# Kernel tuning notes

Hardware: AMD Instinct MI355X
Metric: run time of the kernel (lower is better)

The kernel has to match this reference:

```python
import jax, jax.numpy as jnp
import numpy as np

DIM = 1024
NUM_HEADS = 16
HEAD_DIM = DIM // NUM_HEADS
BATCH = 4
SEQ = 2048
EPS = 1e-6


def rotate_half(x):
    # interleaved-pair rotation: (..., d) -> view (..., d//2, 2), swap with sign
    x = x.reshape(*x.shape[:-1], -1, 2)
    x1, x2 = jnp.split(x, 2, axis=-1)  # each (..., d//2, 1)
    x = jnp.concatenate([-x2, x1], axis=-1)
    return x.reshape(*x.shape[:-2], -1)


def apply_rope(x, cos, sin):
    # x: [B,S,H,D], cos/sin: [S,D]
    cos = cos[None, :, None, :].astype(x.dtype)
    sin = sin[None, :, None, :].astype(x.dtype)
    return x * cos + rotate_half(x) * sin


def rms_norm(x, w):
    var = jnp.mean(jnp.square(x), axis=-1, keepdims=True)
    return x * jax.lax.rsqrt(var + EPS) * w


def setup_inputs() -> dict:
    key = jax.random.key(0)
    ks = jax.random.split(key, 8)
    s = 0.02
    return {
        "x": jax.random.normal(ks[0], (BATCH, SEQ, DIM), jnp.float32),
        "rope_cos": jnp.cos(jnp.arange(SEQ, dtype=jnp.float32)[:, None] *
                            (1.0 / (10000.0 ** (jnp.repeat(jnp.arange(HEAD_DIM // 2, dtype=jnp.float32), 2) * 2 / HEAD_DIM)))[None, :]),
        "rope_sin": jnp.sin(jnp.arange(SEQ, dtype=jnp.float32)[:, None] *
                            (1.0 / (10000.0 ** (jnp.repeat(jnp.arange(HEAD_DIM // 2, dtype=jnp.float32), 2) * 2 / HEAD_DIM)))[None, :]),
        "qkv_w": jax.random.normal(ks[1], (3 * DIM, DIM), jnp.float32) * s,
        "qkv_b": jax.random.normal(ks[2], (3 * DIM,), jnp.float32) * s,
        "proj_w": jax.random.normal(ks[3], (DIM, DIM), jnp.float32) * s,
        "proj_b": jax.random.normal(ks[4], (DIM,), jnp.float32) * s,
        "q_norm_w": jnp.ones((HEAD_DIM,), jnp.float32),
        "k_norm_w": jnp.ones((HEAD_DIM,), jnp.float32),
    }


def reference(x, rope_cos, rope_sin, qkv_w, qkv_b, proj_w, proj_b, q_norm_w, k_norm_w):
    B, S, C = x.shape
    H, D = NUM_HEADS, HEAD_DIM
    qkv = x @ qkv_w.T + qkv_b                      # [B,S,3C]
    qkv = qkv.reshape(B, S, 3, H, D)
    q, k, v = qkv[:, :, 0], qkv[:, :, 1], qkv[:, :, 2]  # [B,S,H,D]
    q = apply_rope(rms_norm(q, q_norm_w), rope_cos, rope_sin)
    k = apply_rope(rms_norm(k, k_norm_w), rope_cos, rope_sin)
    scale = 1.0 / np.sqrt(D).astype(np.float32)
    attn = jnp.einsum('bqhd,bkhd->bhqk', q.astype(jnp.float32), k.astype(jnp.float32))
    attn = jax.nn.softmax(attn * scale, axis=-1).astype(x.dtype)
    out = jnp.einsum('bhqk,bkhd->bqhd', attn, v).reshape(B, S, C)
    return out @ proj_w.T + proj_b
```

## Files before the change

### kernel.cpp

```cpp
#include <hip/hip_runtime.h>
#include <math.h>
#include <type_traits>

#define DIM 1024
#define NH 16
#define HD 64
#define BATCH 4
#define SEQ 2048
#define EPS 1e-6f

typedef __attribute__((ext_vector_type(8))) short short8;
typedef __attribute__((ext_vector_type(4))) short short4v;
typedef __attribute__((ext_vector_type(4))) float float4v;

__device__ inline unsigned short f2bf(float f) {
    unsigned u = __float_as_uint(f);
    u += 0x7FFF + ((u >> 16) & 1);
    return (unsigned short)(u >> 16);
}
__device__ inline float bf2f(unsigned short b) {
    return __uint_as_float(((unsigned)b) << 16);
}
__device__ inline unsigned pk2bf(float lo, float hi) {
    unsigned ul = __float_as_uint(lo) + 0x8000u;
    unsigned uh = __float_as_uint(hi) + 0x8000u;
    return __builtin_amdgcn_perm(uh, ul, 0x07060302u);
}
__device__ inline unsigned short hu2bf(float f) {
    return (unsigned short)((__float_as_uint(f) + 0x8000u) >> 16);
}

#if __has_builtin(__builtin_amdgcn_mfma_f32_16x16x16bf16_1k)
__device__ inline float4v mfma16(short4v a, short4v b, float4v c) {
    return __builtin_amdgcn_mfma_f32_16x16x16bf16_1k(a, b, c, 0, 0, 0);
}
#elif __has_builtin(__builtin_amdgcn_mfma_f32_16x16x16_bf16)
__device__ inline float4v mfma16(short4v a, short4v b, float4v c) {
    return __builtin_amdgcn_mfma_f32_16x16x16_bf16(a, b, c, 0, 0, 0);
}
#else
__device__ inline float4v mfma16(short4v a, short4v b, float4v c) {
    asm volatile("v_mfma_f32_16x16x16_bf16 %0, %1, %2, %0\n\ts_nop 4"
                 : "+v"(c) : "v"(a), "v"(b));
    return c;
}
#endif

#define GLDS16(gp, lp) __builtin_amdgcn_global_load_lds( \
    (const __attribute__((address_space(1))) void*)(gp), \
    (__attribute__((address_space(3))) void*)(lp), 16, 0, 0)

__global__ __launch_bounds__(256) void cast_f32_bf16(
    const float* __restrict__ src, unsigned short* __restrict__ dst, int n4)
{
    int i = blockIdx.x * 256 + threadIdx.x;
    if (i >= n4) return;
    float4 f = ((const float4*)src)[i];
    ushort4 o;
    o.x = f2bf(f.x); o.y = f2bf(f.y); o.z = f2bf(f.z); o.w = f2bf(f.w);
    ((ushort4*)dst)[i] = o;
}

__global__ __launch_bounds__(256) void prep_cs(
    const float* __restrict__ cos_t, const float* __restrict__ sin_t,
    unsigned* __restrict__ csT)
{
    int tid = blockIdx.x * 256 + threadIdx.x;
    int d = tid & 63, s = tid >> 6;
    float c = cos_t[s * 64 + d], sn = sin_t[s * 64 + d];
    csT[d * SEQ + s] = ((unsigned)f2bf(sn) << 16) | f2bf(c);
}

__global__ __launch_bounds__(256) void gemm_qkv_fused(
    const unsigned short* __restrict__ A, const unsigned short* __restrict__ W,
    const float* __restrict__ bias, const unsigned* __restrict__ csT,
    const float* __restrict__ qw, const float* __restrict__ kw,
    unsigned short* __restrict__ q, unsigned short* __restrict__ k,
    unsigned short* __restrict__ vt)
{
    __shared__ __align__(16) unsigned short As[128 * 32];
    __shared__ __align__(16) unsigned short Bs[128 * 32];

    const int t    = threadIdx.x;
    const int lane = t & 63;
    const int w    = t >> 6;
    const int row0 = blockIdx.y * 128;
    const int col0 = blockIdx.x * 128;
    const int wr   = (w & 1) * 64;
    const int wc   = (w >> 1) * 64;
    const int cl   = lane & 15;
    const int quad = lane >> 4;

    float4v acc[4][4];
#pragma unroll
    for (int i = 0; i < 4; ++i)
#pragma unroll
        for (int j = 0; j < 4; ++j) acc[i][j] = (float4v){0.f, 0.f, 0.f, 0.f};

    const int off1 = t * 16, off2 = 4096 + t * 16;
    const int r1 = off1 >> 6, c1 = off1 & 63;
    const int r2 = off2 >> 6, c2 = off2 & 63;
    const char* Ab = (const char*)A + (long)row0 * DIM * 2;
    const char* Wb = (const char*)W + (long)col0 * DIM * 2;
    const long  ks = DIM * 2;

    for (int k0 = 0; k0 < DIM; k0 += 32) {
        const long kb = (long)k0 * 2;
        GLDS16(Ab + (long)r1 * ks + kb + c1, (char*)As + off1);
        GLDS16(Ab + (long)r2 * ks + kb + c2, (char*)As + off2);
        GLDS16(Wb + (long)r1 * ks + kb + c1, (char*)Bs + off1);
        GLDS16(Wb + (long)r2 * ks + kb + c2, (char*)Bs + off2);
        __syncthreads();

        short8 af[4], bfr[4];
#pragma unroll
        for (int i = 0; i < 4; ++i)
            af[i] = *(const short8*)&As[(wr + i * 16 + cl) * 32 + quad * 8];
#pragma unroll
        for (int j = 0; j < 4; ++j)
            bfr[j] = *(const short8*)&Bs[(wc + j * 16 + cl) * 32 + quad * 8];
#pragma unroll
        for (int i = 0; i < 4; ++i)
#pragma unroll
            for (int j = 0; j < 4; ++j)
                acc[i][j] = __builtin_amdgcn_mfma_f32_16x16x32_bf16(af[i], bfr[j], acc[i][j], 0, 0, 0);
        __syncthreads();
    }

    const int gcol  = col0 + wc;
    const int b     = row0 >> 11;
    const int srow0 = (row0 & 2047) + wr;

    float bj[4];
#pragma unroll
    for (int j = 0; j < 4; ++j) bj[j] = bias[gcol + j * 16 + cl];

    if (gcol < 2 * DIM) {
        const bool isq = (gcol < DIM);
        const int  h   = (isq ? gcol : gcol - DIM) >> 6;
        const float* nw = isq ? qw : kw;
        const float scale = isq ? 0.125f : 1.0f;
        unsigned short* dst = (isq ? q : k) + ((long)(b * NH + h) * SEQ) * 64;

#pragma unroll
        for (int i = 0; i < 4; ++i)
#pragma unroll
            for (int j = 0; j < 4; ++j)
#pragma unroll
                for (int r = 0; r < 4; ++r) acc[i][j][r] += bj[j];

        float rinv[4][4];
#pragma unroll
        for (int i = 0; i < 4; ++i)
#pragma unroll
            for (int r = 0; r < 4; ++r) {
                float ss = acc[i][0][r] * acc[i][0][r];
                ss = fmaf(acc[i][1][r], acc[i][1][r], ss);
                ss = fmaf(acc[i][2][r], acc[i][2][r], ss);
                ss = fmaf(acc[i][3][r], acc[i][3][r], ss);
                ss += __shfl_xor(ss, 1, 64);
                ss += __shfl_xor(ss, 2, 64);
                ss += __shfl_xor(ss, 4, 64);
                ss += __shfl_xor(ss, 8, 64);
                rinv[i][r] = rsqrtf(ss * (1.f / 64.f) + EPS) * scale;
            }

        float nwj[4];
#pragma unroll
        for (int j = 0; j < 4; ++j) nwj[j] = nw[j * 16 + cl];

#pragma unroll
        for (int i = 0; i < 4; ++i) {
            const int sb = srow0 + i * 16 + quad * 4;
#pragma unroll
            for (int j = 0; j < 4; ++j) {
                const int d = j * 16 + cl;
                uint4 u4 = *(const uint4*)(csT + (long)d * SEQ + sb);
#pragma unroll
                for (int r = 0; r < 4; ++r) {
                    float qn = acc[i][j][r] * rinv[i][r] * nwj[j];
                    float p  = __shfl_xor(qn, 1, 64);
                    float pr = (cl & 1) ? p : -p;
                    unsigned u = (r == 0) ? u4.x : (r == 1) ? u4.y : (r == 2) ? u4.z : u4.w;
                    float c  = bf2f((unsigned short)(u & 0xffff));
                    float sn = bf2f((unsigned short)(u >> 16));
                    float ov = fmaf(qn, c, pr * sn);
                    dst[(long)(sb + r) * 64 + d] = hu2bf(ov);
                }
            }
        }
    } else {
        const int h = (gcol - 2 * DIM) >> 6;
        unsigned short* vdst = vt + (long)(b * NH + h) * SEQ * 64
                                  + (long)(srow0 >> 6) * 4096;
#pragma unroll
        for (int j = 0; j < 4; ++j)
#pragma unroll
            for (int ip = 0; ip < 2; ++ip) {
                const int i0 = 2 * ip;
                uint4 st;
                st.x = pk2bf(acc[i0][j][0] + bj[j],     acc[i0][j][1] + bj[j]);
                st.y = pk2bf(acc[i0][j][2] + bj[j],     acc[i0][j][3] + bj[j]);
                st.z = pk2bf(acc[i0 + 1][j][0] + bj[j], acc[i0 + 1][j][1] + bj[j]);
                st.w = pk2bf(acc[i0 + 1][j][2] + bj[j], acc[i0 + 1][j][3] + bj[j]);
                *(uint4*)(vdst + (j * 2 + ip) * 512 + lane * 8) = st;
            }
    }
}

template <typename OT>
__global__ __launch_bounds__(256) void gemm_mfma_bt(
    const unsigned short* __restrict__ A, const unsigned short* __restrict__ W,
    const float* __restrict__ bias, OT* __restrict__ C,
    int M, int N, int K)
{
    __shared__ __align__(16) unsigned short As[128 * 32];
    __shared__ __align__(16) unsigned short Bs[128 * 32];

    const int t    = threadIdx.x;
    const int lane = t & 63;
    const int w    = t >> 6;
    const int row0 = blockIdx.y * 128;
    const int col0 = blockIdx.x * 128;
    const int wr   = (w & 1) * 64;
    const int wc   = (w >> 1) * 64;

    float4v acc[4][4];
#pragma unroll
    for (int i = 0; i < 4; ++i)
#pragma unroll
        for (int j = 0; j < 4; ++j) acc[i][j] = (float4v){0.f, 0.f, 0.f, 0.f};

    const int off1 = t * 16, off2 = 4096 + t * 16;
    const int r1 = off1 >> 6, c1 = off1 & 63;
    const int r2 = off2 >> 6, c2 = off2 & 63;
    const char* Ab = (const char*)A + (long)row0 * K * 2;
    const char* Wb = (const char*)W + (long)col0 * K * 2;
    const long  ks = (long)K * 2;

    for (int k0 = 0; k0 < K; k0 += 32) {
        const long kb = (long)k0 * 2;
        GLDS16(Ab + (long)r1 * ks + kb + c1, (char*)As + off1);
        GLDS16(Ab + (long)r2 * ks + kb + c2, (char*)As + off2);
        GLDS16(Wb + (long)r1 * ks + kb + c1, (char*)Bs + off1);
        GLDS16(Wb + (long)r2 * ks + kb + c2, (char*)Bs + off2);
        __syncthreads();

        short8 af[4], bfr[4];
#pragma unroll
        for (int i = 0; i < 4; ++i)
            af[i] = *(const short8*)&As[(wr + i * 16 + (lane & 15)) * 32 + (lane >> 4) * 8];
#pragma unroll
        for (int j = 0; j < 4; ++j)
            bfr[j] = *(const short8*)&Bs[(wc + j * 16 + (lane & 15)) * 32 + (lane >> 4) * 8];
#pragma unroll
        for (int i = 0; i < 4; ++i)
#pragma unroll
            for (int j = 0; j < 4; ++j)
                acc[i][j] = __builtin_amdgcn_mfma_f32_16x16x32_bf16(af[i], bfr[j], acc[i][j], 0, 0, 0);
        __syncthreads();
    }

    const int qd = lane >> 4, cl = lane & 15;
#pragma unroll
    for (int j = 0; j < 4; ++j) {
        const int col = col0 + wc + j * 16 + cl;
        const float bj = bias[col];
#pragma unroll
        for (int i = 0; i < 4; ++i) {
            const long rr = row0 + wr + i * 16 + qd * 4;
#pragma unroll
            for (int r = 0; r < 4; ++r) {
                float val = acc[i][j][r] + bj;
                if constexpr (std::is_same<OT, unsigned short>::value)
                    C[(rr + r) * (long)N + col] = f2bf(val);
                else
                    C[(rr + r) * (long)N + col] = val;
            }
        }
    }
}

__global__ __launch_bounds__(256) void flash_mfma(
    const unsigned short* __restrict__ q, const unsigned short* __restrict__ k,
    const unsigned short* __restrict__ vt, unsigned short* __restrict__ out)
{
    __shared__ __align__(16) unsigned short Qs[2][64 * 32];
    __shared__ __align__(16) unsigned short Ks[2][64 * 32];
    __shared__ __align__(16) unsigned short Vts[64 * 64];

    const int t    = threadIdx.x;
    const int lane = t & 63;
    const int w    = t >> 6;
    const int bh   = blockIdx.y;
    const int b    = bh >> 4;
    const int h    = bh & 15;
    const int q0   = blockIdx.x * 64;
    const int cl   = lane & 15;
    const int quad = lane >> 4;

    const char* qb  = (const char*)(q  + (long)bh * SEQ * 64);
    const char* kb  = (const char*)(k  + (long)bh * SEQ * 64);
    const char* vtb = (const char*)(vt + (long)bh * SEQ * 64);

    {
        const int off = t * 16, row = off >> 6, cb = off & 63;
#pragma unroll
        for (int hf = 0; hf < 2; ++hf)
            GLDS16(qb + (long)(q0 + row) * 128 + hf * 64 + cb, (char*)Qs[hf] + off);
    }
    __syncthreads();

    short8 aq[2];
#pragma unroll
    for (int c = 0; c < 2; ++c)
        aq[c] = *(const short8*)&Qs[c][(w * 16 + cl) * 32 + quad * 8];

    float4v o[4];
    float lacc = 0.f;
#pragma unroll
    for (int i = 0; i < 4; ++i) o[i] = (float4v){0.f, 0.f, 0.f, 0.f};

    const int soff = t * 16, srow = soff >> 6, scb = soff & 63;

    for (int kt = 0; kt < SEQ / 64; ++kt) {
#pragma unroll
        for (int hf = 0; hf < 2; ++hf)
            GLDS16(kb + (long)(kt * 64 + srow) * 128 + hf * 64 + scb, (char*)Ks[hf] + soff);
        GLDS16(vtb + (long)kt * 8192 + 0    + t * 16, (char*)Vts + t * 16);
        GLDS16(vtb + (long)kt * 8192 + 4096 + t * 16, (char*)Vts + 4096 + t * 16);
        __syncthreads();

        float4v sa[4];
#pragma unroll
        for (int j = 0; j < 4; ++j) {
            short8 a0 = *(const short8*)&Ks[0][(j * 16 + cl) * 32 + quad * 8];
            short8 a1 = *(const short8*)&Ks[1][(j * 16 + cl) * 32 + quad * 8];
            float4v z = (float4v){0.f, 0.f, 0.f, 0.f};
            z = __builtin_amdgcn_mfma_f32_16x16x32_bf16(a0, aq[0], z, 0, 0, 0);
            sa[j] = __builtin_amdgcn_mfma_f32_16x16x32_bf16(a1, aq[1], z, 0, 0, 0);
        }

        short4v pa[4];
#pragma unroll
        for (int j = 0; j < 4; ++j) {
            float p0 = __expf(sa[j][0]), p1 = __expf(sa[j][1]);
            float p2 = __expf(sa[j][2]), p3 = __expf(sa[j][3]);
            lacc += (p0 + p1) + (p2 + p3);
            unsigned lo = pk2bf(p0, p1), hi = pk2bf(p2, p3);
            pa[j] = __builtin_bit_cast(short4v, ((unsigned long long)hi << 32) | lo);
        }

#pragma unroll
        for (int fi = 0; fi < 4; ++fi) {
#pragma unroll
            for (int fjp = 0; fjp < 2; ++fjp) {
                short8 vv = *(const short8*)&Vts[(fi * 2 + fjp) * 512 + lane * 8];
                short4v va = __builtin_shufflevector(vv, vv, 0, 1, 2, 3);
                short4v vb = __builtin_shufflevector(vv, vv, 4, 5, 6, 7);
                o[fi] = mfma16(va, pa[2 * fjp], o[fi]);
                o[fi] = mfma16(vb, pa[2 * fjp + 1], o[fi]);
            }
        }
        __syncthreads();
    }

    lacc += __shfl_xor(lacc, 16, 64);
    lacc += __shfl_xor(lacc, 32, 64);
    const float inv = 1.f / lacc;

    unsigned short* orow = out + ((long)b * SEQ + q0 + w * 16 + cl) * DIM + h * 64;
#pragma unroll
    for (int i = 0; i < 4; ++i) {
        unsigned lo = pk2bf(o[i][0] * inv, o[i][1] * inv);
        unsigned hi = pk2bf(o[i][2] * inv, o[i][3] * inv);
        ushort4 st = __builtin_bit_cast(ushort4, ((unsigned long long)hi << 32) | lo);
        *(ushort4*)(orow + i * 16 + quad * 4) = st;
    }
}

extern "C" void kernel_launch(void* const* d_in, const int* in_sizes, int n_in,
                              void* d_out, int out_size, void* d_ws, size_t ws_size,
                              hipStream_t stream)
{
    const float* x        = (const float*)d_in[0];
    const float* rope_cos = (const float*)d_in[1];
    const float* rope_sin = (const float*)d_in[2];
    const float* qkv_w    = (const float*)d_in[3];
    const float* qkv_b    = (const float*)d_in[4];
    const float* proj_w   = (const float*)d_in[5];
    const float* proj_b   = (const float*)d_in[6];
    const float* q_norm_w = (const float*)d_in[7];
    const float* k_norm_w = (const float*)d_in[8];
    float* outp = (float*)d_out;

    const int M = BATCH * SEQ;
    char* p = (char*)d_ws;
    unsigned short* xb    = (unsigned short*)p; p += (long)M * DIM * 2;
    unsigned short* qkvwb = (unsigned short*)p; p += (long)3 * DIM * DIM * 2;
    unsigned short* projwb= (unsigned short*)p; p += (long)DIM * DIM * 2;
    unsigned short* qb    = (unsigned short*)p; p += (long)M * DIM * 2;
    unsigned short* kbuf  = (unsigned short*)p; p += (long)M * DIM * 2;
    unsigned short* vtb   = (unsigned short*)p; p += (long)M * DIM * 2;
    unsigned short* attno = (unsigned short*)p; p += (long)M * DIM * 2;
    unsigned*       csT   = (unsigned*)p;       p += (long)SEQ * 64 * 4;

    prep_cs<<<dim3(SEQ * 64 / 256), 256, 0, stream>>>(rope_cos, rope_sin, csT);
    cast_f32_bf16<<<dim3((M * DIM / 4) / 256), 256, 0, stream>>>(x, xb, M * DIM / 4);
    cast_f32_bf16<<<dim3((3 * DIM * DIM / 4) / 256), 256, 0, stream>>>(qkv_w, qkvwb, 3 * DIM * DIM / 4);
    cast_f32_bf16<<<dim3((DIM * DIM / 4) / 256), 256, 0, stream>>>(proj_w, projwb, DIM * DIM / 4);

    gemm_qkv_fused<<<dim3(3 * DIM / 128, M / 128), 256, 0, stream>>>(
        xb, qkvwb, qkv_b, csT, q_norm_w, k_norm_w, qb, kbuf, vtb);

    flash_mfma<<<dim3(SEQ / 64, BATCH * NH), 256, 0, stream>>>(qb, kbuf, vtb, attno);

    gemm_mfma_bt<float><<<dim3(DIM / 128, M / 128), 256, 0, stream>>>(
        attno, projwb, proj_b, outp, M, DIM, DIM);
}
```

Measured before the change: 347.7 us.

## Fuse prep kernels, permute QKV weight rows for lane-local RoPE, widen attention tile

Merges the four preprocessing launches into one kernel. That kernel also permutes the Q/K rows of the QKV weight so each lane holds both elements of a RoPE pair, which removes the cross-lane shuffle and allows packed 32-bit stores. Q is pre-scaled by log2(e)/sqrt(d) so softmax uses exp2. The flash kernel now handles 128 query rows per block with two query groups per wave, so each K/V tile is reused twice. The row sum is computed by an MFMA against a ones vector. This raises register pressure and risks some accuracy, because the row sum is taken from bf16-rounded probabilities and no max subtraction is done.

```diff
diff --git a/kernel.cpp b/kernel.cpp
--- a/kernel.cpp
+++ b/kernel.cpp
@@ -26,9 +26,12 @@
     unsigned uh = __float_as_uint(hi) + 0x8000u;
     return __builtin_amdgcn_perm(uh, ul, 0x07060302u);
 }
-__device__ inline unsigned short hu2bf(float f) {
-    return (unsigned short)((__float_as_uint(f) + 0x8000u) >> 16);
-}
+
+#if __has_builtin(__builtin_amdgcn_exp2f)
+#define EXP2F(x) __builtin_amdgcn_exp2f(x)
+#else
+#define EXP2F(x) exp2f(x)
+#endif
 
 #if __has_builtin(__builtin_amdgcn_mfma_f32_16x16x16bf16_1k)
 __device__ inline float4v mfma16(short4v a, short4v b, float4v c) {
@@ -50,30 +53,48 @@
     (const __attribute__((address_space(1))) void*)(gp), \
     (__attribute__((address_space(3))) void*)(lp), 16, 0, 0)
 
-__global__ __launch_bounds__(256) void cast_f32_bf16(
-    const float* __restrict__ src, unsigned short* __restrict__ dst, int n4)
+__global__ __launch_bounds__(256) void prep_all(
+    const float* __restrict__ x, const float* __restrict__ qkv_w,
+    const float* __restrict__ proj_w,
+    const float* __restrict__ cos_t, const float* __restrict__ sin_t,
+    unsigned short* __restrict__ xb, unsigned short* __restrict__ qkvwb,
+    unsigned short* __restrict__ projwb, unsigned* __restrict__ csP)
 {
-    int i = blockIdx.x * 256 + threadIdx.x;
-    if (i >= n4) return;
-    float4 f = ((const float4*)src)[i];
-    ushort4 o;
-    o.x = f2bf(f.x); o.y = f2bf(f.y); o.z = f2bf(f.z); o.w = f2bf(f.w);
-    ((ushort4*)dst)[i] = o;
-}
-
-__global__ __launch_bounds__(256) void prep_cs(
-    const float* __restrict__ cos_t, const float* __restrict__ sin_t,
-    unsigned* __restrict__ csT)
-{
-    int tid = blockIdx.x * 256 + threadIdx.x;
-    int d = tid & 63, s = tid >> 6;
-    float c = cos_t[s * 64 + d], sn = sin_t[s * 64 + d];
-    csT[d * SEQ + s] = ((unsigned)f2bf(sn) << 16) | f2bf(c);
+    const int bid = blockIdx.x;
+    if (bid < 8192) {
+        int i = bid * 256 + threadIdx.x;
+        float4 f = ((const float4*)x)[i];
+        ushort4 o;
+        o.x = f2bf(f.x); o.y = f2bf(f.y); o.z = f2bf(f.z); o.w = f2bf(f.w);
+        ((ushort4*)xb)[i] = o;
+    } else if (bid < 8192 + 3072) {
+        const int rn = bid - 8192;
+        int ro = rn;
+        if (rn < 2048) {
+            const int head = rn >> 6, c = rn & 63, j = c >> 4, cl = c & 15;
+            ro = (head << 6) + ((j & 1) + 2 * cl + 32 * (j >> 1));
+        }
+        float4 f = ((const float4*)(qkv_w + (long)ro * DIM))[threadIdx.x];
+        ushort4 o;
+        o.x = f2bf(f.x); o.y = f2bf(f.y); o.z = f2bf(f.z); o.w = f2bf(f.w);
+        ((ushort4*)(qkvwb + (long)rn * DIM))[threadIdx.x] = o;
+    } else if (bid < 8192 + 3072 + 1024) {
+        int i = (bid - 11264) * 256 + threadIdx.x;
+        float4 f = ((const float4*)proj_w)[i];
+        ushort4 o;
+        o.x = f2bf(f.x); o.y = f2bf(f.y); o.z = f2bf(f.z); o.w = f2bf(f.w);
+        ((ushort4*)projwb)[i] = o;
+    } else {
+        int i = (bid - 12288) * 256 + threadIdx.x;
+        int a = i >> 11, s = i & 2047;
+        float c = cos_t[s * 64 + 2 * a], sn = sin_t[s * 64 + 2 * a];
+        csP[a * SEQ + s] = ((unsigned)f2bf(sn) << 16) | f2bf(c);
+    }
 }
 
 __global__ __launch_bounds__(256) void gemm_qkv_fused(
     const unsigned short* __restrict__ A, const unsigned short* __restrict__ W,
-    const float* __restrict__ bias, const unsigned* __restrict__ csT,
+    const float* __restrict__ bias, const unsigned* __restrict__ csP,
     const float* __restrict__ qw, const float* __restrict__ kw,
     unsigned short* __restrict__ q, unsigned short* __restrict__ k,
     unsigned short* __restrict__ vt)
@@ -131,23 +152,23 @@
     const int b     = row0 >> 11;
     const int srow0 = (row0 & 2047) + wr;
 
-    float bj[4];
-#pragma unroll
-    for (int j = 0; j < 4; ++j) bj[j] = bias[gcol + j * 16 + cl];
-
     if (gcol < 2 * DIM) {
         const bool isq = (gcol < DIM);
         const int  h   = (isq ? gcol : gcol - DIM) >> 6;
         const float* nw = isq ? qw : kw;
-        const float scale = isq ? 0.125f : 1.0f;
-        unsigned short* dst = (isq ? q : k) + ((long)(b * NH + h) * SEQ) * 64;
-
+        const float scale = isq ? 0.180336880f : 1.0f;
+        unsigned short* dst = (isq ? q : k) + (long)(b * NH + h) * SEQ * 64;
+
+        float bjv[4];
+#pragma unroll
+        for (int j = 0; j < 4; ++j)
+            bjv[j] = bias[gcol + (j & 1) + 2 * cl + 32 * (j >> 1)];
 #pragma unroll
         for (int i = 0; i < 4; ++i)
 #pragma unroll
             for (int j = 0; j < 4; ++j)
 #pragma unroll
-                for (int r = 0; r < 4; ++r) acc[i][j][r] += bj[j];
+                for (int r = 0; r < 4; ++r) acc[i][j][r] += bjv[j];
 
         float rinv[4][4];
 #pragma unroll
@@ -165,32 +186,34 @@
                 rinv[i][r] = rsqrtf(ss * (1.f / 64.f) + EPS) * scale;
             }
 
-        float nwj[4];
-#pragma unroll
-        for (int j = 0; j < 4; ++j) nwj[j] = nw[j * 16 + cl];
+        const float nwe[2] = { nw[2 * cl],     nw[32 + 2 * cl] };
+        const float nwo[2] = { nw[2 * cl + 1], nw[33 + 2 * cl] };
 
 #pragma unroll
         for (int i = 0; i < 4; ++i) {
             const int sb = srow0 + i * 16 + quad * 4;
 #pragma unroll
-            for (int j = 0; j < 4; ++j) {
-                const int d = j * 16 + cl;
-                uint4 u4 = *(const uint4*)(csT + (long)d * SEQ + sb);
+            for (int jp = 0; jp < 2; ++jp) {
+                uint4 cs4 = *(const uint4*)(csP + (long)(jp * 16 + cl) * SEQ + sb);
 #pragma unroll
                 for (int r = 0; r < 4; ++r) {
-                    float qn = acc[i][j][r] * rinv[i][r] * nwj[j];
-                    float p  = __shfl_xor(qn, 1, 64);
-                    float pr = (cl & 1) ? p : -p;
-                    unsigned u = (r == 0) ? u4.x : (r == 1) ? u4.y : (r == 2) ? u4.z : u4.w;
+                    float g  = rinv[i][r];
+                    float xe = acc[i][2 * jp][r]     * g * nwe[jp];
+                    float xo = acc[i][2 * jp + 1][r] * g * nwo[jp];
+                    unsigned u = (r == 0) ? cs4.x : (r == 1) ? cs4.y : (r == 2) ? cs4.z : cs4.w;
                     float c  = bf2f((unsigned short)(u & 0xffff));
                     float sn = bf2f((unsigned short)(u >> 16));
-                    float ov = fmaf(qn, c, pr * sn);
-                    dst[(long)(sb + r) * 64 + d] = hu2bf(ov);
+                    float oe = fmaf(xe, c, -(xo * sn));
+                    float oo = fmaf(xo, c,   xe * sn);
+                    *(unsigned*)(dst + (long)(sb + r) * 64 + jp * 32 + 2 * cl) = pk2bf(oe, oo);
                 }
             }
         }
     } else {
         const int h = (gcol - 2 * DIM) >> 6;
+        float bjv[4];
+#pragma unroll
+        for (int j = 0; j < 4; ++j) bjv[j] = bias[gcol + j * 16 + cl];
         unsigned short* vdst = vt + (long)(b * NH + h) * SEQ * 64
                                   + (long)(srow0 >> 6) * 4096;
 #pragma unroll
@@ -199,20 +222,18 @@
             for (int ip = 0; ip < 2; ++ip) {
                 const int i0 = 2 * ip;
                 uint4 st;
-                st.x = pk2bf(acc[i0][j][0] + bj[j],     acc[i0][j][1] + bj[j]);
-                st.y = pk2bf(acc[i0][j][2] + bj[j],     acc[i0][j][3] + bj[j]);
-                st.z = pk2bf(acc[i0 + 1][j][0] + bj[j], acc[i0 + 1][j][1] + bj[j]);
-                st.w = pk2bf(acc[i0 + 1][j][2] + bj[j], acc[i0 + 1][j][3] + bj[j]);
+                st.x = pk2bf(acc[i0][j][0] + bjv[j],     acc[i0][j][1] + bjv[j]);
+                st.y = pk2bf(acc[i0][j][2] + bjv[j],     acc[i0][j][3] + bjv[j]);
+                st.z = pk2bf(acc[i0 + 1][j][0] + bjv[j], acc[i0 + 1][j][1] + bjv[j]);
+                st.w = pk2bf(acc[i0 + 1][j][2] + bjv[j], acc[i0 + 1][j][3] + bjv[j]);
                 *(uint4*)(vdst + (j * 2 + ip) * 512 + lane * 8) = st;
             }
     }
 }
 
-template <typename OT>
-__global__ __launch_bounds__(256) void gemm_mfma_bt(
+__global__ __launch_bounds__(256) void gemm_proj(
     const unsigned short* __restrict__ A, const unsigned short* __restrict__ W,
-    const float* __restrict__ bias, OT* __restrict__ C,
-    int M, int N, int K)
+    const float* __restrict__ bias, float* __restrict__ C)
 {
     __shared__ __align__(16) unsigned short As[128 * 32];
     __shared__ __align__(16) unsigned short Bs[128 * 32];
@@ -234,11 +255,11 @@
     const int off1 = t * 16, off2 = 4096 + t * 16;
     const int r1 = off1 >> 6, c1 = off1 & 63;
     const int r2 = off2 >> 6, c2 = off2 & 63;
-    const char* Ab = (const char*)A + (long)row0 * K * 2;
-    const char* Wb = (const char*)W + (long)col0 * K * 2;
-    const long  ks = (long)K * 2;
-
-    for (int k0 = 0; k0 < K; k0 += 32) {
+    const char* Ab = (const char*)A + (long)row0 * DIM * 2;
+    const char* Wb = (const char*)W + (long)col0 * DIM * 2;
+    const long  ks = DIM * 2;
+
+    for (int k0 = 0; k0 < DIM; k0 += 32) {
         const long kb = (long)k0 * 2;
         GLDS16(Ab + (long)r1 * ks + kb + c1, (char*)As + off1);
         GLDS16(Ab + (long)r2 * ks + kb + c2, (char*)As + off2);
@@ -270,13 +291,8 @@
         for (int i = 0; i < 4; ++i) {
             const long rr = row0 + wr + i * 16 + qd * 4;
 #pragma unroll
-            for (int r = 0; r < 4; ++r) {
-                float val = acc[i][j][r] + bj;
-                if constexpr (std::is_same<OT, unsigned short>::value)
-                    C[(rr + r) * (long)N + col] = f2bf(val);
-                else
-                    C[(rr + r) * (long)N + col] = val;
-            }
+            for (int r = 0; r < 4; ++r)
+                C[(rr + r) * (long)DIM + col] = acc[i][j][r] + bj;
         }
     }
 }
@@ -285,7 +301,7 @@
     const unsigned short* __restrict__ q, const unsigned short* __restrict__ k,
     const unsigned short* __restrict__ vt, unsigned short* __restrict__ out)
 {
-    __shared__ __align__(16) unsigned short Qs[2][64 * 32];
+    __shared__ __align__(16) unsigned short Qs[2][128 * 32];
     __shared__ __align__(16) unsigned short Ks[2][64 * 32];
     __shared__ __align__(16) unsigned short Vts[64 * 64];
 
@@ -295,7 +311,7 @@
     const int bh   = blockIdx.y;
     const int b    = bh >> 4;
     const int h    = bh & 15;
-    const int q0   = blockIdx.x * 64;
+    const int q0   = blockIdx.x * 128;
     const int cl   = lane & 15;
     const int quad = lane >> 4;
 
@@ -303,23 +319,32 @@
     const char* kb  = (const char*)(k  + (long)bh * SEQ * 64);
     const char* vtb = (const char*)(vt + (long)bh * SEQ * 64);
 
-    {
-        const int off = t * 16, row = off >> 6, cb = off & 63;
+#pragma unroll
+    for (int rd = 0; rd < 2; ++rd) {
+        const int off = rd * 4096 + t * 16;
+        const int row = off >> 6, cb = off & 63;
 #pragma unroll
         for (int hf = 0; hf < 2; ++hf)
             GLDS16(qb + (long)(q0 + row) * 128 + hf * 64 + cb, (char*)Qs[hf] + off);
     }
     __syncthreads();
 
-    short8 aq[2];
-#pragma unroll
-    for (int c = 0; c < 2; ++c)
-        aq[c] = *(const short8*)&Qs[c][(w * 16 + cl) * 32 + quad * 8];
-
-    float4v o[4];
-    float lacc = 0.f;
-#pragma unroll
-    for (int i = 0; i < 4; ++i) o[i] = (float4v){0.f, 0.f, 0.f, 0.f};
+    short8 aq[2][2];
+#pragma unroll
+    for (int qg = 0; qg < 2; ++qg)
+#pragma unroll
+        for (int hf = 0; hf < 2; ++hf)
+            aq[qg][hf] = *(const short8*)&Qs[hf][(w * 32 + qg * 16 + cl) * 32 + quad * 8];
+
+    const short4v ones = (short4v){(short)0x3F80, (short)0x3F80, (short)0x3F80, (short)0x3F80};
+
+    float4v o[2][4], o4[2];
+#pragma unroll
+    for (int qg = 0; qg < 2; ++qg) {
+        o4[qg] = (float4v){0.f, 0.f, 0.f, 0.f};
+#pragma unroll
+        for (int i = 0; i < 4; ++i) o[qg][i] = (float4v){0.f, 0.f, 0.f, 0.f};
+    }
 
     const int soff = t * 16, srow = soff >> 6, scb = soff & 63;
 
@@ -327,28 +352,26 @@
 #pragma unroll
         for (int hf = 0; hf < 2; ++hf)
             GLDS16(kb + (long)(kt * 64 + srow) * 128 + hf * 64 + scb, (char*)Ks[hf] + soff);
-        GLDS16(vtb + (long)kt * 8192 + 0    + t * 16, (char*)Vts + t * 16);
+        GLDS16(vtb + (long)kt * 8192 + t * 16,        (char*)Vts + t * 16);
         GLDS16(vtb + (long)kt * 8192 + 4096 + t * 16, (char*)Vts + 4096 + t * 16);
         __syncthreads();
 
-        float4v sa[4];
+        short4v pa[2][4];
 #pragma unroll
         for (int j = 0; j < 4; ++j) {
             short8 a0 = *(const short8*)&Ks[0][(j * 16 + cl) * 32 + quad * 8];
             short8 a1 = *(const short8*)&Ks[1][(j * 16 + cl) * 32 + quad * 8];
-            float4v z = (float4v){0.f, 0.f, 0.f, 0.f};
-            z = __builtin_amdgcn_mfma_f32_16x16x32_bf16(a0, aq[0], z, 0, 0, 0);
-            sa[j] = __builtin_amdgcn_mfma_f32_16x16x32_bf16(a1, aq[1], z, 0, 0, 0);
-        }
-
-        short4v pa[4];
-#pragma unroll
-        for (int j = 0; j < 4; ++j) {
-            float p0 = __expf(sa[j][0]), p1 = __expf(sa[j][1]);
-            float p2 = __expf(sa[j][2]), p3 = __expf(sa[j][3]);
-            lacc += (p0 + p1) + (p2 + p3);
-            unsigned lo = pk2bf(p0, p1), hi = pk2bf(p2, p3);
-            pa[j] = __builtin_bit_cast(short4v, ((unsigned long long)hi << 32) | lo);
+#pragma unroll
+            for (int qg = 0; qg < 2; ++qg) {
+                float4v z = (float4v){0.f, 0.f, 0.f, 0.f};
+                z = __builtin_amdgcn_mfma_f32_16x16x32_bf16(a0, aq[qg][0], z, 0, 0, 0);
+                float4v s = __builtin_amdgcn_mfma_f32_16x16x32_bf16(a1, aq[qg][1], z, 0, 0, 0);
+                float p0 = EXP2F(s[0]), p1 = EXP2F(s[1]);
+                float p2 = EXP2F(s[2]), p3 = EXP2F(s[3]);
+                unsigned lo = pk2bf(p0, p1), hi = pk2bf(p2, p3);
+                pa[qg][j] = __builtin_bit_cast(short4v, ((unsigned long long)hi << 32) | lo);
+                o4[qg] = mfma16(ones, pa[qg][j], o4[qg]);
+            }
         }
 
 #pragma unroll
@@ -358,24 +381,27 @@
                 short8 vv = *(const short8*)&Vts[(fi * 2 + fjp) * 512 + lane * 8];
                 short4v va = __builtin_shufflevector(vv, vv, 0, 1, 2, 3);
                 short4v vb = __builtin_shufflevector(vv, vv, 4, 5, 6, 7);
-                o[fi] = mfma16(va, pa[2 * fjp], o[fi]);
-                o[fi] = mfma16(vb, pa[2 * fjp + 1], o[fi]);
+#pragma unroll
+                for (int qg = 0; qg < 2; ++qg) {
+                    o[qg][fi] = mfma16(va, pa[qg][2 * fjp],     o[qg][fi]);
+                    o[qg][fi] = mfma16(vb, pa[qg][2 * fjp + 1], o[qg][fi]);
+                }
             }
         }
         __syncthreads();
     }
 
-    lacc += __shfl_xor(lacc, 16, 64);
-    lacc += __shfl_xor(lacc, 32, 64);
-    const float inv = 1.f / lacc;
-
-    unsigned short* orow = out + ((long)b * SEQ + q0 + w * 16 + cl) * DIM + h * 64;
-#pragma unroll
-    for (int i = 0; i < 4; ++i) {
-        unsigned lo = pk2bf(o[i][0] * inv, o[i][1] * inv);
-        unsigned hi = pk2bf(o[i][2] * inv, o[i][3] * inv);
-        ushort4 st = __builtin_bit_cast(ushort4, ((unsigned long long)hi << 32) | lo);
-        *(ushort4*)(orow + i * 16 + quad * 4) = st;
+#pragma unroll
+    for (int qg = 0; qg < 2; ++qg) {
+        const float inv = 1.f / o4[qg][0];
+        unsigned short* orow = out + ((long)b * SEQ + q0 + w * 32 + qg * 16 + cl) * DIM + h * 64;
+#pragma unroll
+        for (int i = 0; i < 4; ++i) {
+            unsigned lo = pk2bf(o[qg][i][0] * inv, o[qg][i][1] * inv);
+            unsigned hi = pk2bf(o[qg][i][2] * inv, o[qg][i][3] * inv);
+            ushort4 st = __builtin_bit_cast(ushort4, ((unsigned long long)hi << 32) | lo);
+            *(ushort4*)(orow + i * 16 + quad * 4) = st;
+        }
     }
 }
 
@@ -403,18 +429,16 @@
     unsigned short* kbuf  = (unsigned short*)p; p += (long)M * DIM * 2;
     unsigned short* vtb   = (unsigned short*)p; p += (long)M * DIM * 2;
     unsigned short* attno = (unsigned short*)p; p += (long)M * DIM * 2;
-    unsigned*       csT   = (unsigned*)p;       p += (long)SEQ * 64 * 4;
-
-    prep_cs<<<dim3(SEQ * 64 / 256), 256, 0, stream>>>(rope_cos, rope_sin, csT);
-    cast_f32_bf16<<<dim3((M * DIM / 4) / 256), 256, 0, stream>>>(x, xb, M * DIM / 4);
-    cast_f32_bf16<<<dim3((3 * DIM * DIM / 4) / 256), 256, 0, stream>>>(qkv_w, qkvwb, 3 * DIM * DIM / 4);
-    cast_f32_bf16<<<dim3((DIM * DIM / 4) / 256), 256, 0, stream>>>(proj_w, projwb, DIM * DIM / 4);
+    unsigned*       csP   = (unsigned*)p;       p += (long)32 * SEQ * 4;
+
+    prep_all<<<dim3(12544), 256, 0, stream>>>(
+        x, qkv_w, proj_w, rope_cos, rope_sin, xb, qkvwb, projwb, csP);
 
     gemm_qkv_fused<<<dim3(3 * DIM / 128, M / 128), 256, 0, stream>>>(
-        xb, qkvwb, qkv_b, csT, q_norm_w, k_norm_w, qb, kbuf, vtb);
-
-    flash_mfma<<<dim3(SEQ / 64, BATCH * NH), 256, 0, stream>>>(qb, kbuf, vtb, attno);
-
-    gemm_mfma_bt<float><<<dim3(DIM / 128, M / 128), 256, 0, stream>>>(
-        attno, projwb, proj_b, outp, M, DIM, DIM);
-}
+        xb, qkvwb, qkv_b, csP, q_norm_w, k_norm_w, qb, kbuf, vtb);
+
+    flash_mfma<<<dim3(SEQ / 128, BATCH * NH), 256, 0, stream>>>(qb, kbuf, vtb, attno);
+
+    gemm_proj<<<dim3(DIM / 128, M / 128), 256, 0, stream>>>(
+        attno, projwb, proj_b, outp);
+}
```

After: 302.9 us. 1.15x faster.
